# Performance work log

Hardware: AMD Instinct MI355X
Metric: run time of the kernel (lower is better)

The kernel has to match this reference:

```python
import jax, jax.numpy as jnp
import numpy as np

B, D, T = 32, 6, 2048
FH, ENC, H, CONF, NC, K = 128, 128, 256, 64, 10, 5


def setup_inputs() -> dict:
    key = jax.random.key(0)
    ks = iter(jax.random.split(key, 40))
    n = lambda shape, s=0.05: jax.random.normal(next(ks), shape, dtype=jnp.float32) * s
    inp = {
        'M': jax.random.normal(next(ks), (B, D, T), dtype=jnp.float32),
        # causal conv frontend (4 dilated convs, kernel 5)
        'conv_w0': n((FH, D, K)), 'conv_b0': n((FH,)),
        'conv_w1': n((FH, FH, K)), 'conv_b1': n((FH,)),
        'conv_w2': n((FH, FH, K)), 'conv_b2': n((FH,)),
        'conv_w3': n((FH, FH, K)), 'conv_b3': n((FH,)),
        # encoder projection
        'enc_w': n((ENC, FH)), 'enc_b': n((ENC,)),
        # selective state space
        'A': n((H, H), 0.01), 'ip_w': n((H, ENC)), 'ip_b': n((H,)),
        'state_bias': jnp.zeros((H,), jnp.float32),
        'op_w': n((H, H)), 'op_b': n((H,)),
        # classifier head
        'cls_w1': n((256, H)), 'cls_b1': n((256,)),
        'cls_w2': n((NC, 256)), 'cls_b2': n((NC,)),
        # metanet: 2*D -> 64 -> 128 -> confound_dim
        'mn_w1': n((64, 2 * D)), 'mn_b1': n((64,)),
        'mn_w2': n((128, 64)), 'mn_b2': n((128,)),
        'mn_w3': n((CONF, 128)), 'mn_b3': n((CONF,)),
        # frontdoor: confound_dim -> 128 -> ssm_hidden
        'fd_w1': n((128, CONF)), 'fd_b1': n((128,)),
        'fd_w2': n((H, 128)), 'fd_b2': n((H,)),
    }
    return inp


def _causal_conv(x, w, b, d):
    # x: (B,C,T), w: (O,I,K). pad-left (K-1)*d == pad-both + trim-right in torch code
    y = jax.lax.conv_general_dilated(
        x, w, window_strides=(1,), padding=[((w.shape[2] - 1) * d, 0)],
        rhs_dilation=(d,), dimension_numbers=('NCH', 'OIH', 'NCH'))
    return jax.nn.relu(y + b[None, :, None])


def reference(M, conv_w0, conv_b0, conv_w1, conv_b1, conv_w2, conv_b2, conv_w3, conv_b3,
              enc_w, enc_b, A, ip_w, ip_b, state_bias, op_w, op_b,
              cls_w1, cls_b1, cls_w2, cls_b2,
              mn_w1, mn_b1, mn_w2, mn_b2, mn_w3, mn_b3,
              fd_w1, fd_b1, fd_w2, fd_b2):
    # frontend: 4 causal dilated convs with ReLU
    out = M
    for w, b, d in ((conv_w0, conv_b0, 1), (conv_w1, conv_b1, 2),
                    (conv_w2, conv_b2, 4), (conv_w3, conv_b3, 8)):
        out = _causal_conv(out, w, b, d)
    feat = jnp.einsum('bct,ec->bte', out, enc_w) + enc_b  # (B,T,ENC)
    # SSM: precompute input projection, then sequential scan over T
    u = jnp.einsum('bte,he->bth', feat, ip_w) + ip_b + state_bias  # (B,T,H)

    def step(h, ut):
        h = jax.nn.gelu(h @ A.T + ut, approximate=False)
        return h, h

    h0 = jnp.zeros((M.shape[0], A.shape[0]), M.dtype)
    _, hs = jax.lax.scan(step, h0, jnp.swapaxes(u, 0, 1))  # hs: (T,B,H)
    ssm_out = jnp.einsum('tbh,gh->btg', hs, op_w) + op_b  # (B,T,H)
    pooled = ssm_out.mean(axis=1)  # (B,H)
    logits = jax.nn.relu(pooled @ cls_w1.T + cls_b1) @ cls_w2.T + cls_b2
    # confounder summary: mean & unbiased std over time
    s = jnp.concatenate([M.mean(axis=2), jnp.std(M, axis=2, ddof=1)], axis=1)
    z = jax.nn.relu(s @ mn_w1.T + mn_b1)
    z = jax.nn.relu(z @ mn_w2.T + mn_b2)
    conf_hat = z @ mn_w3.T + mn_b3
    adj = jax.nn.relu(conf_hat @ fd_w1.T + fd_b1) @ fd_w2.T + fd_b2
    corrected = pooled - adj
    return (logits, pooled, corrected, conf_hat)
```

## Files before the change

kernel.cpp:

```cpp
#include <hip/hip_runtime.h>
#include <cmath>


typedef __bf16 bf16_t;
typedef bf16_t bf16x8 __attribute__((ext_vector_type(8)));
typedef float f32x4 __attribute__((ext_vector_type(4)));

__device__ __forceinline__ f32x4 mfma16(bf16x8 a, bf16x8 b, f32x4 c) {
  return __builtin_amdgcn_mfma_f32_16x16x32_bf16(a, b, c, 0, 0, 0);
}
__device__ __forceinline__ float gelu_f(float x) {
  return 0.5f * x * (1.0f + erff(x * 0.70710678118654752440f));
}

__global__ void k_repack(const float* __restrict__ w0, const float* __restrict__ w1,
                         const float* __restrict__ w2, const float* __restrict__ w3,
                         bf16_t* __restrict__ wb0, bf16_t* __restrict__ wb1,
                         bf16_t* __restrict__ wb2, bf16_t* __restrict__ wb3) {
  int idx = blockIdx.x * 256 + threadIdx.x;
  if (idx < 128 * 32) {
    int o = idx >> 5, k = idx & 31;
    float v = 0.f;
    if (k < 30) { int i = k / 5, kk = k - i * 5; v = w0[(o * 6 + i) * 5 + kk]; }
    wb0[idx] = (bf16_t)v;
    return;
  }
  int e = idx - 128 * 32;
  if (e < 3 * 5 * 128 * 128) {
    int layer = e / (5 * 128 * 128);
    int r = e - layer * (5 * 128 * 128);
    int ks = r / 16384;
    int o = (r >> 7) & 127;
    int i = r & 127;
    const float* w = layer == 0 ? w1 : layer == 1 ? w2 : w3;
    bf16_t* wb = layer == 0 ? wb1 : layer == 1 ? wb2 : wb3;
    wb[r] = (bf16_t)w[(o * 128 + i) * 5 + ks];
  }
}

__global__ void k_wce(const float* __restrict__ ip_w, const float* __restrict__ enc_w,
                      const float* __restrict__ enc_b, const float* __restrict__ ip_b,
                      const float* __restrict__ sbias, bf16_t* __restrict__ wce,
                      float* __restrict__ bce) {
  int h = blockIdx.x, c = threadIdx.x;
  float s = 0.f;
  for (int e = 0; e < 128; ++e) s += ip_w[h * 128 + e] * enc_w[e * 128 + c];
  wce[h * 128 + c] = (bf16_t)s;
  if (c == 0) {
    float bv = 0.f;
    for (int e = 0; e < 128; ++e) bv += ip_w[h * 128 + e] * enc_b[e];
    bce[h] = bv + ip_b[h] + sbias[h];
  }
}

__global__ __launch_bounds__(256) void k_conv0(const float* __restrict__ M,
                                               const bf16_t* __restrict__ wb0,
                                               const float* __restrict__ b0,
                                               bf16_t* __restrict__ out) {
  __shared__ float raw[6][136];
  __shared__ bf16_t Xe[128 * 40];
  const int tid = threadIdx.x;
  const int b = blockIdx.y, t0 = blockIdx.x * 128;
  for (int id = tid; id < 6 * 132; id += 256) {
    int i = id / 132, j = id - i * 132;
    int t = t0 - 4 + j;
    raw[i][j] = (t >= 0) ? M[((size_t)b * 6 + i) * 2048 + t] : 0.f;
  }
  __syncthreads();
  for (int id = tid; id < 128 * 32; id += 256) {
    int tl = id >> 5, k = id & 31;
    float v = 0.f;
    if (k < 30) { int i = k / 5, kk = k - i * 5; v = raw[i][tl + kk]; }
    Xe[tl * 40 + k] = (bf16_t)v;
  }
  __syncthreads();
  const int w = tid >> 6, lane = tid & 63, q = lane >> 4, l15 = lane & 15;
  const int k0 = q * 8;
  const f32x4 z4 = {0.f, 0.f, 0.f, 0.f};
  f32x4 acc[2][8];
#pragma unroll
  for (int mt = 0; mt < 2; ++mt)
#pragma unroll
    for (int nt = 0; nt < 8; ++nt) acc[mt][nt] = z4;
  bf16x8 af[2];
#pragma unroll
  for (int mt = 0; mt < 2; ++mt)
    af[mt] = *(const bf16x8*)&Xe[(w * 32 + mt * 16 + l15) * 40 + k0];
#pragma unroll
  for (int nt = 0; nt < 8; ++nt) {
    bf16x8 bf = *(const bf16x8*)&wb0[(nt * 16 + l15) * 32 + k0];
#pragma unroll
    for (int mt = 0; mt < 2; ++mt) acc[mt][nt] = mfma16(af[mt], bf, acc[mt][nt]);
  }
#pragma unroll
  for (int nt = 0; nt < 8; ++nt) {
    const int o = nt * 16 + l15;
    const float bias = b0[o];
#pragma unroll
    for (int mt = 0; mt < 2; ++mt) {
#pragma unroll
      for (int r = 0; r < 4; ++r) {
        int t = t0 + w * 32 + mt * 16 + q * 4 + r;
        float v = acc[mt][nt][r] + bias;
        out[((size_t)b * 2048 + t) * 128 + o] = (bf16_t)(v > 0.f ? v : 0.f);
      }
    }
  }
}

template <int DIL>
__global__ __launch_bounds__(256) void k_conv(const bf16_t* __restrict__ in,
                                              const bf16_t* __restrict__ wb,
                                              const float* __restrict__ bias,
                                              bf16_t* __restrict__ out) {
  __shared__ bf16_t Xs[160 * 136];
  const int tid = threadIdx.x;
  const int b = blockIdx.y, t0 = blockIdx.x * 128;
  const bf16_t* src = in + (size_t)b * 2048 * 128;
  for (int id = tid; id < 160 * 16; id += 256) {
    int r = id >> 4, ck = id & 15;
    int t = t0 + r - 32;
    int4 v = make_int4(0, 0, 0, 0);
    if (t >= 0) v = *(const int4*)(src + (size_t)t * 128 + ck * 8);
    *(int4*)&Xs[r * 136 + ck * 8] = v;
  }
  __syncthreads();
  const int w = tid >> 6, lane = tid & 63, q = lane >> 4, l15 = lane & 15;
  const f32x4 z4 = {0.f, 0.f, 0.f, 0.f};
  f32x4 acc[2][8];
#pragma unroll
  for (int mt = 0; mt < 2; ++mt)
#pragma unroll
    for (int nt = 0; nt < 8; ++nt) acc[mt][nt] = z4;
#pragma unroll
  for (int ks = 0; ks < 5; ++ks) {
    const int shift = (4 - ks) * DIL;
#pragma unroll
    for (int kt = 0; kt < 4; ++kt) {
      const int k0 = kt * 32 + q * 8;
      bf16x8 af[2];
#pragma unroll
      for (int mt = 0; mt < 2; ++mt)
        af[mt] = *(const bf16x8*)&Xs[(32 + w * 32 + mt * 16 + l15 - shift) * 136 + k0];
#pragma unroll
      for (int nt = 0; nt < 8; ++nt) {
        bf16x8 bf = *(const bf16x8*)&wb[((size_t)ks * 128 + nt * 16 + l15) * 128 + k0];
#pragma unroll
        for (int mt = 0; mt < 2; ++mt) acc[mt][nt] = mfma16(af[mt], bf, acc[mt][nt]);
      }
    }
  }
#pragma unroll
  for (int nt = 0; nt < 8; ++nt) {
    const int o = nt * 16 + l15;
    const float bv = bias[o];
#pragma unroll
    for (int mt = 0; mt < 2; ++mt) {
#pragma unroll
      for (int r = 0; r < 4; ++r) {
        int t = t0 + w * 32 + mt * 16 + q * 4 + r;
        float v = acc[mt][nt][r] + bv;
        out[((size_t)b * 2048 + t) * 128 + o] = (bf16_t)(v > 0.f ? v : 0.f);
      }
    }
  }
}

__global__ __launch_bounds__(256) void k_ugemm(const bf16_t* __restrict__ in,
                                               const bf16_t* __restrict__ wce,
                                               const float* __restrict__ bce,
                                               bf16_t* __restrict__ u) {
  __shared__ bf16_t Xs[128 * 136];
  const int tid = threadIdx.x;
  const int b = blockIdx.y, t0 = blockIdx.x * 128, hh = blockIdx.z;
  const bf16_t* src = in + (size_t)b * 2048 * 128;
  for (int id = tid; id < 128 * 16; id += 256) {
    int r = id >> 4, ck = id & 15;
    *(int4*)&Xs[r * 136 + ck * 8] = *(const int4*)(src + (size_t)(t0 + r) * 128 + ck * 8);
  }
  __syncthreads();
  const int w = tid >> 6, lane = tid & 63, q = lane >> 4, l15 = lane & 15;
  const f32x4 z4 = {0.f, 0.f, 0.f, 0.f};
  f32x4 acc[2][8];
#pragma unroll
  for (int mt = 0; mt < 2; ++mt)
#pragma unroll
    for (int nt = 0; nt < 8; ++nt) acc[mt][nt] = z4;
#pragma unroll
  for (int kt = 0; kt < 4; ++kt) {
    const int k0 = kt * 32 + q * 8;
    bf16x8 af[2];
#pragma unroll
    for (int mt = 0; mt < 2; ++mt)
      af[mt] = *(const bf16x8*)&Xs[(w * 32 + mt * 16 + l15) * 136 + k0];
#pragma unroll
    for (int nt = 0; nt < 8; ++nt) {
      bf16x8 bf = *(const bf16x8*)&wce[((size_t)hh * 128 + nt * 16 + l15) * 128 + k0];
#pragma unroll
      for (int mt = 0; mt < 2; ++mt) acc[mt][nt] = mfma16(af[mt], bf, acc[mt][nt]);
    }
  }
#pragma unroll
  for (int nt = 0; nt < 8; ++nt) {
    const int h = hh * 128 + nt * 16 + l15;
    const float bv = bce[h];
#pragma unroll
    for (int mt = 0; mt < 2; ++mt) {
#pragma unroll
      for (int r = 0; r < 4; ++r) {
        int t = t0 + w * 32 + mt * 16 + q * 4 + r;
        u[((size_t)b * 2048 + t) * 256 + h] = (bf16_t)(acc[mt][nt][r] + bv);
      }
    }
  }
}

__global__ __launch_bounds__(256, 1) void k_scan(const float* __restrict__ Am,
                                                 const bf16_t* __restrict__ u,
                                                 float* __restrict__ hbarOut) {
  __shared__ bf16_t hb[2][256];
  const int b = blockIdx.x;
  const int tid = threadIdx.x;
  const int w = tid >> 6, lane = tid & 63, q = lane >> 4, l15 = lane & 15;

  bf16x8 bfr[4][8];
#pragma unroll
  for (int nt = 0; nt < 4; ++nt) {
    const int c = w * 64 + nt * 16 + l15;
#pragma unroll
    for (int kt = 0; kt < 8; ++kt) {
      const float* ap = Am + (size_t)c * 256 + kt * 32 + q * 8;
      f32x4 p0 = *(const f32x4*)ap;
      f32x4 p1 = *(const f32x4*)(ap + 4);
      bf16x8 v;
      v[0] = (bf16_t)p0[0]; v[1] = (bf16_t)p0[1]; v[2] = (bf16_t)p0[2]; v[3] = (bf16_t)p0[3];
      v[4] = (bf16_t)p1[0]; v[5] = (bf16_t)p1[1]; v[6] = (bf16_t)p1[2]; v[7] = (bf16_t)p1[3];
      bfr[nt][kt] = v;
    }
  }
  hb[0][tid] = (bf16_t)0.f;
  hb[1][tid] = (bf16_t)0.f;
  const bf16_t* up = u + (size_t)b * 2048 * 256 + tid;
  float hbar = 0.f;
  float ucur = (float)up[0];
  __syncthreads();

  int rd = 0;
  const f32x4 z4 = {0.f, 0.f, 0.f, 0.f};
  for (int t = 0; t < 2048; ++t) {
    float unxt = (t < 2047) ? (float)up[(size_t)(t + 1) * 256] : 0.f;
    f32x4 acc[4] = {z4, z4, z4, z4};
#pragma unroll
    for (int kt = 0; kt < 8; ++kt) {
      bf16x8 af = *(const bf16x8*)&hb[rd][kt * 32 + q * 8];
#pragma unroll
      for (int nt = 0; nt < 4; ++nt) acc[nt] = mfma16(af, bfr[nt][kt], acc[nt]);
    }
    float y = (q == 0) ? acc[0][0] : (q == 1) ? acc[1][0] : (q == 2) ? acc[2][0] : acc[3][0];
    float g = gelu_f(y + ucur);
    hbar += g;
    hb[rd ^ 1][tid] = (bf16_t)g;
    __syncthreads();
    ucur = unxt;
    rd ^= 1;
  }
  hbarOut[b * 256 + tid] = hbar * (1.f / 2048.f);
}

__global__ void k_meta1(const float* __restrict__ M, float* __restrict__ stats) {
  const int c = blockIdx.x, b = blockIdx.y, tid = threadIdx.x;
  const float* p = M + ((size_t)b * 6 + c) * 2048;
  float s = 0.f, ss = 0.f;
  for (int t = tid; t < 2048; t += 256) { float v = p[t]; s += v; ss += v * v; }
  for (int o = 32; o > 0; o >>= 1) { s += __shfl_down(s, o, 64); ss += __shfl_down(ss, o, 64); }
  __shared__ float as_[4], ass_[4];
  const int w = tid >> 6, lane = tid & 63;
  if (lane == 0) { as_[w] = s; ass_[w] = ss; }
  __syncthreads();
  if (tid == 0) {
    s = as_[0] + as_[1] + as_[2] + as_[3];
    ss = ass_[0] + ass_[1] + ass_[2] + ass_[3];
    float mean = s * (1.f / 2048.f);
    float var = (ss - 2048.f * mean * mean) * (1.f / 2047.f);
    if (var < 0.f) var = 0.f;
    stats[b * 12 + c] = mean;
    stats[b * 12 + 6 + c] = sqrtf(var);
  }
}

__global__ void k_meta2(const float* __restrict__ stats,
                        const float* __restrict__ w1, const float* __restrict__ b1,
                        const float* __restrict__ w2, const float* __restrict__ b2,
                        const float* __restrict__ w3, const float* __restrict__ b3,
                        const float* __restrict__ f1, const float* __restrict__ fb1,
                        const float* __restrict__ f2, const float* __restrict__ fb2,
                        float* __restrict__ out, float* __restrict__ adj) {
  const int b = blockIdx.x, tid = threadIdx.x;
  __shared__ float s[12], z1[64], z2[128], ch[64], a1[128];
  if (tid < 12) s[tid] = stats[b * 12 + tid];
  __syncthreads();
  if (tid < 64) {
    float v = b1[tid];
    for (int e = 0; e < 12; ++e) v += w1[tid * 12 + e] * s[e];
    z1[tid] = v > 0.f ? v : 0.f;
  }
  __syncthreads();
  if (tid < 128) {
    float v = b2[tid];
    for (int e = 0; e < 64; ++e) v += w2[tid * 64 + e] * z1[e];
    z2[tid] = v > 0.f ? v : 0.f;
  }
  __syncthreads();
  if (tid < 64) {
    float v = b3[tid];
    for (int e = 0; e < 128; ++e) v += w3[tid * 128 + e] * z2[e];
    ch[tid] = v;
    out[16704 + b * 64 + tid] = v;
  }
  __syncthreads();
  if (tid < 128) {
    float v = fb1[tid];
    for (int e = 0; e < 64; ++e) v += f1[tid * 64 + e] * ch[e];
    a1[tid] = v > 0.f ? v : 0.f;
  }
  __syncthreads();
  {
    float v = fb2[tid];
    for (int e = 0; e < 128; ++e) v += f2[tid * 128 + e] * a1[e];
    adj[b * 256 + tid] = v;
  }
}

__global__ void k_head(const float* __restrict__ hbar, const float* __restrict__ op_w,
                       const float* __restrict__ op_b, const float* __restrict__ cw1,
                       const float* __restrict__ cb1, const float* __restrict__ cw2,
                       const float* __restrict__ cb2, const float* __restrict__ adj,
                       float* __restrict__ out) {
  const int b = blockIdx.x, g = threadIdx.x;
  __shared__ float hs[256], ps[256], hid[256];
  hs[g] = hbar[b * 256 + g];
  __syncthreads();
  float v = op_b[g];
  for (int h = 0; h < 256; ++h) v += op_w[g * 256 + h] * hs[h];
  out[320 + b * 256 + g] = v;
  out[8512 + b * 256 + g] = v - adj[b * 256 + g];
  ps[g] = v;
  __syncthreads();
  float hv = cb1[g];
  for (int h = 0; h < 256; ++h) hv += cw1[g * 256 + h] * ps[h];
  hid[g] = hv > 0.f ? hv : 0.f;
  __syncthreads();
  if (g < 10) {
    float lv = cb2[g];
    for (int h = 0; h < 256; ++h) lv += cw2[g * 256 + h] * hid[h];
    out[b * 10 + g] = lv;
  }
}

extern "C" void kernel_launch(void* const* d_in, const int* in_sizes, int n_in,
                              void* d_out, int out_size, void* d_ws, size_t ws_size,
                              hipStream_t stream) {
  (void)in_sizes; (void)n_in; (void)out_size; (void)ws_size;
  const float* M    = (const float*)d_in[0];
  const float* w0   = (const float*)d_in[1];  const float* b0  = (const float*)d_in[2];
  const float* w1   = (const float*)d_in[3];  const float* b1  = (const float*)d_in[4];
  const float* w2   = (const float*)d_in[5];  const float* b2  = (const float*)d_in[6];
  const float* w3   = (const float*)d_in[7];  const float* b3  = (const float*)d_in[8];
  const float* encw = (const float*)d_in[9];  const float* encb = (const float*)d_in[10];
  const float* Am   = (const float*)d_in[11];
  const float* ipw  = (const float*)d_in[12]; const float* ipb = (const float*)d_in[13];
  const float* sb   = (const float*)d_in[14];
  const float* opw  = (const float*)d_in[15]; const float* opb = (const float*)d_in[16];
  const float* cw1  = (const float*)d_in[17]; const float* cb1 = (const float*)d_in[18];
  const float* cw2  = (const float*)d_in[19]; const float* cb2 = (const float*)d_in[20];
  const float* mw1  = (const float*)d_in[21]; const float* mb1 = (const float*)d_in[22];
  const float* mw2  = (const float*)d_in[23]; const float* mb2 = (const float*)d_in[24];
  const float* mw3  = (const float*)d_in[25]; const float* mb3 = (const float*)d_in[26];
  const float* fw1  = (const float*)d_in[27]; const float* fb1 = (const float*)d_in[28];
  const float* fw2  = (const float*)d_in[29]; const float* fb2 = (const float*)d_in[30];
  float* out = (float*)d_out;

  char* ws = (char*)d_ws;
  bf16_t* wb0  = (bf16_t*)(ws + 0);
  bf16_t* wb1  = (bf16_t*)(ws + 8192);
  bf16_t* wb2  = (bf16_t*)(ws + 172032);
  bf16_t* wb3  = (bf16_t*)(ws + 335872);
  bf16_t* wce  = (bf16_t*)(ws + 499712);
  float*  bce  = (float*) (ws + 565248);
  float*  hbar = (float*) (ws + 566272);
  float*  adj  = (float*) (ws + 599040);
  float*  stats= (float*) (ws + 631808);
  bf16_t* actA = (bf16_t*)(ws + 633856);
  bf16_t* actB = (bf16_t*)(ws + 17411072);
  bf16_t* u    = (bf16_t*)(ws + 34188288);

  k_repack<<<976, 256, 0, stream>>>(w0, w1, w2, w3, wb0, wb1, wb2, wb3);
  k_wce<<<256, 128, 0, stream>>>(ipw, encw, encb, ipb, sb, wce, bce);
  k_conv0<<<dim3(16, 32), 256, 0, stream>>>(M, wb0, b0, actA);
  k_conv<2><<<dim3(16, 32), 256, 0, stream>>>(actA, wb1, b1, actB);
  k_conv<4><<<dim3(16, 32), 256, 0, stream>>>(actB, wb2, b2, actA);
  k_conv<8><<<dim3(16, 32), 256, 0, stream>>>(actA, wb3, b3, actB);
  k_ugemm<<<dim3(16, 32, 2), 256, 0, stream>>>(actB, wce, bce, u);
  k_scan<<<32, 256, 0, stream>>>(Am, u, hbar);
  k_meta1<<<dim3(6, 32), 256, 0, stream>>>(M, stats);
  k_meta2<<<32, 256, 0, stream>>>(stats, mw1, mb1, mw2, mb2, mw3, mb3,
                                  fw1, fb1, fw2, fb2, out, adj);
  k_head<<<32, 256, 0, stream>>>(hbar, opw, opb, cw1, cb1, cw2, cb2, adj, out);
}
```

Measured before the change: 1.653 ms.

## Batch 16 sequences per scan block to fill MFMA tiles, use fast GELU

The sequential SSM scan now processes 16 batch rows per workgroup instead of one. The MFMA N dimension is the batch, so every output lane is useful, where before only one column of each 16x16 tile was kept. Only 2 workgroups are launched instead of 32, trading parallelism for per-step MFMA utilisation. The exact erf GELU is replaced by a tanh approximation built on exp2/rcp. The u stream is prefetched two steps ahead, and the barrier is a raw waitcnt plus s_barrier. The GELU approximation changes numerics slightly, and using only 2 CUs risks long per-step latency.

```diff
diff --git a/kernel.cpp b/kernel.cpp
--- a/kernel.cpp
+++ b/kernel.cpp
@@ -4,6 +4,7 @@
 
 typedef __bf16 bf16_t;
 typedef bf16_t bf16x8 __attribute__((ext_vector_type(8)));
+typedef bf16_t bf16x4 __attribute__((ext_vector_type(4)));
 typedef float f32x4 __attribute__((ext_vector_type(4)));
 
 __device__ __forceinline__ f32x4 mfma16(bf16x8 a, bf16x8 b, f32x4 c) {
@@ -11,6 +12,15 @@
 }
 __device__ __forceinline__ float gelu_f(float x) {
   return 0.5f * x * (1.0f + erff(x * 0.70710678118654752440f));
+}
+__device__ __forceinline__ float gelu_fast(float x) {
+  float x2 = x * x;
+  float inner = x * __builtin_fmaf(0.0356774081f, x2, 0.7978845608f);
+  float e = __builtin_amdgcn_exp2f(inner * -2.88539008f);
+  return x * __builtin_amdgcn_rcpf(1.f + e);
+}
+__device__ __forceinline__ float bf2f(unsigned short us) {
+  return __uint_as_float(((unsigned)us) << 16);
 }
 
 __global__ void k_repack(const float* __restrict__ w0, const float* __restrict__ w1,
@@ -218,53 +228,94 @@
 __global__ __launch_bounds__(256, 1) void k_scan(const float* __restrict__ Am,
                                                  const bf16_t* __restrict__ u,
                                                  float* __restrict__ hbarOut) {
-  __shared__ bf16_t hb[2][256];
-  const int b = blockIdx.x;
+  __shared__ bf16_t Hs[2][16 * 264];
+  const int b0 = blockIdx.x * 16;
   const int tid = threadIdx.x;
   const int w = tid >> 6, lane = tid & 63, q = lane >> 4, l15 = lane & 15;
 
-  bf16x8 bfr[4][8];
-#pragma unroll
-  for (int nt = 0; nt < 4; ++nt) {
-    const int c = w * 64 + nt * 16 + l15;
+  bf16x8 afr[4][8];
+#pragma unroll
+  for (int ft = 0; ft < 4; ++ft) {
+    const int f = w * 64 + ft * 16 + l15;
 #pragma unroll
     for (int kt = 0; kt < 8; ++kt) {
-      const float* ap = Am + (size_t)c * 256 + kt * 32 + q * 8;
+      const float* ap = Am + (size_t)f * 256 + kt * 32 + q * 8;
       f32x4 p0 = *(const f32x4*)ap;
       f32x4 p1 = *(const f32x4*)(ap + 4);
       bf16x8 v;
       v[0] = (bf16_t)p0[0]; v[1] = (bf16_t)p0[1]; v[2] = (bf16_t)p0[2]; v[3] = (bf16_t)p0[3];
       v[4] = (bf16_t)p1[0]; v[5] = (bf16_t)p1[1]; v[6] = (bf16_t)p1[2]; v[7] = (bf16_t)p1[3];
-      bfr[nt][kt] = v;
-    }
-  }
-  hb[0][tid] = (bf16_t)0.f;
-  hb[1][tid] = (bf16_t)0.f;
-  const bf16_t* up = u + (size_t)b * 2048 * 256 + tid;
-  float hbar = 0.f;
-  float ucur = (float)up[0];
+      afr[ft][kt] = v;
+    }
+  }
+  for (int i = tid; i < 2 * 16 * 264 / 2; i += 256) ((int*)Hs)[i] = 0;
+
+  const bf16_t* up = u + ((size_t)(b0 + l15) * 2048) * 256 + w * 64 + q * 4;
+  ushort4 uc[4], un[4];
+#pragma unroll
+  for (int ft = 0; ft < 4; ++ft) uc[ft] = *(const ushort4*)(up + ft * 16);
+#pragma unroll
+  for (int ft = 0; ft < 4; ++ft) un[ft] = *(const ushort4*)(up + 256 + ft * 16);
+
+  float hbar[4][4];
+#pragma unroll
+  for (int ft = 0; ft < 4; ++ft)
+#pragma unroll
+    for (int r = 0; r < 4; ++r) hbar[ft][r] = 0.f;
+
+  const int rdbase = l15 * 264 + q * 8;
+  const int wrbase = l15 * 264 + w * 64 + q * 4;
   __syncthreads();
 
   int rd = 0;
   const f32x4 z4 = {0.f, 0.f, 0.f, 0.f};
+#pragma unroll 2
   for (int t = 0; t < 2048; ++t) {
-    float unxt = (t < 2047) ? (float)up[(size_t)(t + 1) * 256] : 0.f;
-    f32x4 acc[4] = {z4, z4, z4, z4};
+    bf16x8 hfr[8];
+#pragma unroll
+    for (int kt = 0; kt < 8; ++kt)
+      hfr[kt] = *(const bf16x8*)&Hs[rd][rdbase + kt * 32];
+    ushort4 u2[4];
+    {
+      size_t off = (size_t)(t + 2 <= 2047 ? t + 2 : 2047) * 256;
+#pragma unroll
+      for (int ft = 0; ft < 4; ++ft) u2[ft] = *(const ushort4*)(up + off + ft * 16);
+    }
+    f32x4 a0 = z4, a1 = z4, a2 = z4, a3 = z4;
 #pragma unroll
     for (int kt = 0; kt < 8; ++kt) {
-      bf16x8 af = *(const bf16x8*)&hb[rd][kt * 32 + q * 8];
-#pragma unroll
-      for (int nt = 0; nt < 4; ++nt) acc[nt] = mfma16(af, bfr[nt][kt], acc[nt]);
-    }
-    float y = (q == 0) ? acc[0][0] : (q == 1) ? acc[1][0] : (q == 2) ? acc[2][0] : acc[3][0];
-    float g = gelu_f(y + ucur);
-    hbar += g;
-    hb[rd ^ 1][tid] = (bf16_t)g;
-    __syncthreads();
-    ucur = unxt;
+      a0 = mfma16(afr[0][kt], hfr[kt], a0);
+      a1 = mfma16(afr[1][kt], hfr[kt], a1);
+    }
+#pragma unroll
+    for (int kt = 0; kt < 8; ++kt) {
+      a2 = mfma16(afr[2][kt], hfr[kt], a2);
+      a3 = mfma16(afr[3][kt], hfr[kt], a3);
+    }
+    f32x4 acc[4] = {a0, a1, a2, a3};
+#pragma unroll
+    for (int ft = 0; ft < 4; ++ft) {
+      float g0 = gelu_fast(acc[ft][0] + bf2f(uc[ft].x));
+      float g1 = gelu_fast(acc[ft][1] + bf2f(uc[ft].y));
+      float g2 = gelu_fast(acc[ft][2] + bf2f(uc[ft].z));
+      float g3 = gelu_fast(acc[ft][3] + bf2f(uc[ft].w));
+      hbar[ft][0] += g0; hbar[ft][1] += g1; hbar[ft][2] += g2; hbar[ft][3] += g3;
+      bf16x4 pk;
+      pk[0] = (bf16_t)g0; pk[1] = (bf16_t)g1; pk[2] = (bf16_t)g2; pk[3] = (bf16_t)g3;
+      *(bf16x4*)&Hs[rd ^ 1][wrbase + ft * 16] = pk;
+    }
+    asm volatile("s_waitcnt lgkmcnt(0)\n\ts_barrier" ::: "memory");
+#pragma unroll
+    for (int ft = 0; ft < 4; ++ft) { uc[ft] = un[ft]; un[ft] = u2[ft]; }
     rd ^= 1;
   }
-  hbarOut[b * 256 + tid] = hbar * (1.f / 2048.f);
+#pragma unroll
+  for (int ft = 0; ft < 4; ++ft) {
+    f32x4 vv;
+#pragma unroll
+    for (int r = 0; r < 4; ++r) vv[r] = hbar[ft][r] * (1.f / 2048.f);
+    *(f32x4*)(hbarOut + (size_t)(b0 + l15) * 256 + w * 64 + ft * 16 + q * 4) = vv;
+  }
 }
 
 __global__ void k_meta1(const float* __restrict__ M, float* __restrict__ stats) {
@@ -401,7 +452,7 @@
   k_conv<4><<<dim3(16, 32), 256, 0, stream>>>(actB, wb2, b2, actA);
   k_conv<8><<<dim3(16, 32), 256, 0, stream>>>(actA, wb3, b3, actB);
   k_ugemm<<<dim3(16, 32, 2), 256, 0, stream>>>(actB, wce, bce, u);
-  k_scan<<<32, 256, 0, stream>>>(Am, u, hbar);
+  k_scan<<<2, 256, 0, stream>>>(Am, u, hbar);
   k_meta1<<<dim3(6, 32), 256, 0, stream>>>(M, stats);
   k_meta2<<<32, 256, 0, stream>>>(stats, mw1, mb1, mw2, mb2, mw3, mb3,
                                   fw1, fb1, fw2, fb2, out, adj);
```

After: 2.100 ms. 1.27x slower.
